# Optimization experiments

Hardware: AMD Instinct MI355X
Metric: run time of the kernel (lower is better)

## Reference

```python
import jax, jax.numpy as jnp
import numpy as np

D_MODEL = 1024
D_K = 1024
B, T = 4, 2048


def setup_inputs() -> dict:
    key = jax.random.key(0)
    kx, kq, kk, kv = jax.random.split(key, 4)
    s = 1.0 / np.sqrt(D_MODEL)
    return {
        "x": jax.random.normal(kx, (B, T, D_MODEL), dtype=jnp.float32),
        "W_q": jax.random.normal(kq, (D_MODEL, D_K), dtype=jnp.float32) * s,
        "W_k": jax.random.normal(kk, (D_MODEL, D_K), dtype=jnp.float32) * s,
        "W_v": jax.random.normal(kv, (D_MODEL, D_K), dtype=jnp.float32) * s,
    }


def reference(x, W_q, W_k, W_v):
    # x: (B, T, C); W_*: (C, d_k). Linear(no bias) == x @ W
    q = jnp.einsum('btc,ck->btk', x, W_q)
    k = jnp.einsum('btc,ck->btk', x, W_k)
    v = jnp.einsum('btc,ck->btk', x, W_v)
    d_k = W_q.shape[1]
    scores = jnp.einsum('bqk,bsk->bqs', q, k) / jnp.sqrt(jnp.asarray(d_k, x.dtype))
    T_ = x.shape[1]
    causal = jnp.tril(jnp.ones((T_, T_), dtype=bool))
    scores = jnp.where(causal, scores, jnp.asarray(-jnp.inf, scores.dtype))
    weights = jax.nn.softmax(scores, axis=-1)
    return jnp.einsum('bqs,bsk->bqk', weights, v)
```

## Files before the change

kernel.cpp:

```cpp
#include <hip/hip_runtime.h>
#include <hip/hip_bf16.h>
#include <stdint.h>
#include <math.h>

typedef __bf16 bf16x8 __attribute__((ext_vector_type(8)));
typedef float  f32x4  __attribute__((ext_vector_type(4)));
typedef unsigned int u32x4 __attribute__((ext_vector_type(4)));

__device__ __forceinline__ unsigned short f2bf(float x) {
    union { float f; unsigned u; } v; v.f = x;
    unsigned r = v.u + 0x7fffu + ((v.u >> 16) & 1u);
    return (unsigned short)(r >> 16);
}

__device__ __forceinline__ float bf2f(unsigned short b) {
    union { unsigned u; float f; } v; v.u = ((unsigned)b) << 16; return v.f;
}

__device__ __forceinline__ void async16(const void* g, void* l) {
    __builtin_amdgcn_global_load_lds(
        (const __attribute__((address_space(1))) void*)g,
        (__attribute__((address_space(3))) void*)l,
        16, 0, 0);
}

template <typename OutT, bool KLIMIT, bool VFOLD, int ZMODE, int TN>
__global__ __launch_bounds__(256, (TN == 128) ? 3 : 2) void gemm_bt(
    const unsigned short* __restrict__ A,
    const unsigned short* __restrict__ Bt,
    OutT* __restrict__ C,
    unsigned short* __restrict__ VtOut,
    int M, int N, int K, int lda, int ldb, int ldc,
    int ldvt, int nsplit,
    long long sA, long long sB, long long sC, long long sVt, float scale)
{
    constexpr int NJ   = TN / 32;
    constexpr int BUFE = (TN == 128) ? 8192 : 12288;

    int bn, bm, bz;
    if constexpr (ZMODE == 1) {
        const int o = blockIdx.x, x = o & 7, q = o >> 3;
        bz = x >> 1;
        const int tile = (x & 1) * 96 + q * 4 + blockIdx.z;
        bn = tile / 16; bm = tile % 16;
    } else if constexpr (ZMODE == 2) {
        const int o = blockIdx.x, x = o & 7, q = o >> 3;
        bz = x >> 1;
        const int t = (x & 1) * 68 + q * 4 + blockIdx.z;
        int r = (int)((sqrtf(8.f * (float)t + 1.f) - 1.f) * 0.5f);
        while ((r + 1) * (r + 2) / 2 <= t) r++;
        while (r * (r + 1) / 2 > t) r--;
        bm = r; bn = t - r * (r + 1) / 2;
    } else if constexpr (ZMODE == 3) {
        const int o = blockIdx.x, x = o & 7, q = o >> 3;
        bz = x >> 1;
        const int tile = (x & 1) * 64 + q * 4 + blockIdx.z;
        bn = tile >> 4; bm = 15 - (tile & 15);
    } else {
        bn = blockIdx.x; bm = blockIdx.y; bz = blockIdx.z;
    }

    A  += (long long)bz * sA;
    Bt += (long long)bz * sB;
    C  += (long long)bz * sC;

    const int m0 = bm * 128, n0 = bn * TN;
    const int Keff = KLIMIT ? min(K, (bm + 1) * 128) : K;
    const int nsteps = Keff >> 5;

    __shared__ __align__(16) unsigned short LDS[3 * BUFE];

    const int tid  = threadIdx.x;
    const int w    = tid >> 6, l = tid & 63;
    const int wr   = w >> 1,  wc = w & 1;
    const int lrow = l & 15,  quad = l >> 4;

    f32x4 acc[4][NJ] = {};

    const int cOff = (((l & 3) ^ ((l >> 3) & 3))) * 8;
    const unsigned short* aG0 = A + (long long)(m0 + 32 * w + (l >> 2))      * lda + cOff;
    const unsigned short* aG1 = A + (long long)(m0 + 32 * w + (l >> 2) + 16) * lda + cOff;
    const unsigned short* bG0 = Bt + (long long)(n0 + (TN / 4) * w + (l >> 2))      * ldb + cOff;
    const unsigned short* bG1 = Bt + (long long)(n0 + (TN / 4) * w + (l >> 2) + 16) * ldb + cOff;
    const unsigned short* bG2 = Bt + (long long)(n0 + (TN / 4) * w + (l >> 2) + 32) * ldb + cOff;
    const unsigned short* bG3 = Bt + (long long)(n0 + (TN / 4) * w + (l >> 2) + 48) * ldb + cOff;
    unsigned short* aL = &LDS[w * 1024 + l * 8];
    unsigned short* bL = &LDS[4096 + w * (TN * 8) + l * 8];

    const int sl = (lrow >> 1) & 3;

    auto STG = [&](int s) {
        const int off = (s % 3) * BUFE;
        const int kk  = s * 32;
        async16(aG0 + kk, aL + off);
        async16(aG1 + kk, aL + off + 512);
        async16(bG0 + kk, bL + off);
        async16(bG1 + kk, bL + off + 512);
        if constexpr (TN == 256) {
            async16(bG2 + kk, bL + off + 1024);
            async16(bG3 + kk, bL + off + 1536);
        }
    };

    STG(0);
    if (nsteps > 1) STG(1);

    for (int t = 0; t < nsteps; ++t) {
        if (t + 1 < nsteps) {
            if constexpr (TN == 128) asm volatile("s_waitcnt vmcnt(4)" ::: "memory");
            else                     asm volatile("s_waitcnt vmcnt(6)" ::: "memory");
        } else {
            asm volatile("s_waitcnt vmcnt(0)" ::: "memory");
        }
        __builtin_amdgcn_s_barrier();
        asm volatile("" ::: "memory");

        if (t + 2 < nsteps) STG(t + 2);

        const unsigned short* As = &LDS[(t % 3) * BUFE];
        const unsigned short* Bs = As + 4096;
        bf16x8 af[4], bfr[NJ];
#pragma unroll
        for (int i = 0; i < 4; i++)
            af[i]  = *(const bf16x8*)&As[(wr * 64 + i * 16 + lrow) * 32 + (quad ^ sl) * 8];
#pragma unroll
        for (int j = 0; j < NJ; j++)
            bfr[j] = *(const bf16x8*)&Bs[(wc * (TN / 2) + j * 16 + lrow) * 32 + (quad ^ sl) * 8];
#pragma unroll
        for (int i = 0; i < 4; i++)
#pragma unroll
            for (int j = 0; j < NJ; j++)
                acc[i][j] = __builtin_amdgcn_mfma_f32_16x16x32_bf16(af[i], bfr[j], acc[i][j], 0, 0, 0);
    }

    if constexpr (VFOLD) {
        if (n0 >= nsplit) {
            unsigned short* Vp = VtOut + (long long)bz * sVt;
#pragma unroll
            for (int i = 0; i < 4; i++) {
                const int t = m0 + wr * 64 + i * 16 + quad * 4;
#pragma unroll
                for (int j = 0; j < NJ; j++) {
                    const int d = (n0 - nsplit) + wc * (TN / 2) + j * 16 + lrow;
                    union { unsigned short u[4]; uint2 p; } o;
#pragma unroll
                    for (int r = 0; r < 4; r++) o.u[r] = f2bf(acc[i][j][r] * scale);
                    *(uint2*)(Vp + (long long)d * ldvt + t) = o.p;
                }
            }
            return;
        }
    }

    __syncthreads();

    const int erow = l >> 2, ep = l & 3;

    if constexpr (sizeof(OutT) == 2 && TN == 128) {
        char* eb = (char*)LDS + w * 2288;
#pragma unroll
        for (int i = 0; i < 4; i++) {
#pragma unroll
            for (int j = 0; j < 4; j++)
#pragma unroll
                for (int r = 0; r < 4; r++)
                    *(unsigned short*)(eb + (quad * 4 + r) * 144 + (j * 16 + lrow) * 2) =
                        f2bf(acc[i][j][r] * scale);
            const long long gm = m0 + wr * 64 + i * 16 + erow;
#pragma unroll
            for (int c = 0; c < 2; c++) {
                u32x4 d = *(u32x4*)(eb + erow * 144 + ep * 32 + c * 16);
                *(u32x4*)((unsigned short*)C + gm * ldc + (n0 + wc * 64 + ep * 16 + c * 8)) = d;
            }
        }
    } else if constexpr (sizeof(OutT) == 2 && TN == 256) {
        char* eb = (char*)LDS + w * 4352;
#pragma unroll
        for (int i = 0; i < 4; i++) {
#pragma unroll
            for (int j = 0; j < 8; j++)
#pragma unroll
                for (int r = 0; r < 4; r++)
                    *(unsigned short*)(eb + (quad * 4 + r) * 272 + (j * 16 + lrow) * 2) =
                        f2bf(acc[i][j][r] * scale);
            const long long gm = m0 + wr * 64 + i * 16 + erow;
#pragma unroll
            for (int c = 0; c < 4; c++) {
                u32x4 d = *(u32x4*)(eb + erow * 272 + ep * 64 + c * 16);
                *(u32x4*)((unsigned short*)C + gm * ldc + (n0 + wc * 128 + ep * 32 + c * 8)) = d;
            }
        }
    } else {
        char* eb = (char*)LDS + w * 2304;
#pragma unroll
        for (int i = 0; i < 4; i++) {
            const long long gm = m0 + wr * 64 + i * 16 + erow;
#pragma unroll
            for (int jc = 0; jc < NJ / 2; jc++) {
#pragma unroll
                for (int jj = 0; jj < 2; jj++)
#pragma unroll
                    for (int r = 0; r < 4; r++)
                        *(float*)(eb + (quad * 4 + r) * 144 + (jj * 16 + lrow) * 4) =
                            acc[i][2 * jc + jj][r] * scale;
#pragma unroll
                for (int c = 0; c < 2; c++) {
                    f32x4 d = *(f32x4*)(eb + erow * 144 + ep * 32 + c * 16);
                    *(f32x4*)((float*)C + gm * ldc + (n0 + wc * (TN / 2) + jc * 32 + ep * 8 + c * 4)) = d;
                }
            }
        }
    }
}

__global__ __launch_bounds__(256) void prep_fused(
    const float4* __restrict__ xin, unsigned short* __restrict__ xout, int n4, int nCast,
    const float* __restrict__ W0, const float* __restrict__ W1,
    const float* __restrict__ W2, unsigned short* __restrict__ wout, int n)
{
    const int tid = threadIdx.x;
    if ((int)blockIdx.x < nCast) {
        int i = blockIdx.x * 256 + tid;
        if (i >= n4) return;
        float4 v = xin[i];
        union { unsigned short u[4]; uint2 p; } o;
        o.u[0] = f2bf(v.x); o.u[1] = f2bf(v.y); o.u[2] = f2bf(v.z); o.u[3] = f2bf(v.w);
        *(uint2*)(xout + (long long)i * 4) = o.p;
        return;
    }
    const int bx = blockIdx.x - nCast;
    const int wz = bx >> 10, rem = bx & 1023;
    const int wy = rem >> 5, wx = rem & 31;
    const float* in = (wz == 0) ? W0 : (wz == 1) ? W1 : W2;
    unsigned short* out = wout + (long long)wz * n * n;
    __shared__ float tile[32][33];
    const int tx = tid & 31, ty = tid >> 5;
    const int c0 = wx * 32, r0 = wy * 32;
#pragma unroll
    for (int i = 0; i < 4; i++)
        tile[ty + i * 8][tx] = in[(long long)(r0 + ty + i * 8) * n + c0 + tx];
    __syncthreads();
#pragma unroll
    for (int i = 0; i < 4; i++)
        out[(long long)(c0 + ty + i * 8) * n + r0 + tx] = f2bf(tile[tx][ty + i * 8]);
}

__global__ __launch_bounds__(256) void causal_softmax_bf16(
    const unsigned short* __restrict__ S, unsigned short* __restrict__ P, int T)
{
    const int row = blockIdx.x;
    const int t   = row & (T - 1);
    const int L   = t + 1;
    const unsigned short* s = S + (long long)row * T;
    unsigned short* p = P + (long long)row * T;
    const int tid  = threadIdx.x;
    const int base = tid * 8;

    uint4 raw = *(const uint4*)(s + base);
    unsigned rr[4] = {raw.x, raw.y, raw.z, raw.w};
    float v[8];
#pragma unroll
    for (int k = 0; k < 4; k++) {
        union { unsigned u; float f; } a, b;
        a.u = (rr[k] & 0xFFFFu) << 16;
        b.u = rr[k] & 0xFFFF0000u;
        v[2 * k] = a.f; v[2 * k + 1] = b.f;
    }
    float mx = -3.0e38f;
#pragma unroll
    for (int k = 0; k < 8; k++) {
        if (base + k >= L) v[k] = -3.0e38f;
        mx = fmaxf(mx, v[k]);
    }
#pragma unroll
    for (int off = 32; off; off >>= 1) mx = fmaxf(mx, __shfl_xor(mx, off));
    __shared__ float red[4], red2[4];
    const int wid = tid >> 6, lid = tid & 63;
    if (lid == 0) red[wid] = mx;
    __syncthreads();
    mx = fmaxf(fmaxf(red[0], red[1]), fmaxf(red[2], red[3]));

    float sum = 0.f;
#pragma unroll
    for (int k = 0; k < 8; k++) { v[k] = __expf(v[k] - mx); sum += v[k]; }
#pragma unroll
    for (int off = 32; off; off >>= 1) sum += __shfl_xor(sum, off);
    if (lid == 0) red2[wid] = sum;
    __syncthreads();
    sum = red2[0] + red2[1] + red2[2] + red2[3];
    const float inv = 1.0f / sum;

    union { unsigned short u[8]; uint4 q; } o;
#pragma unroll
    for (int k = 0; k < 8; k++) o.u[k] = f2bf(v[k] * inv);
    *(uint4*)(p + base) = o.q;
}

extern "C" void kernel_launch(void* const* d_in, const int* in_sizes, int n_in,
                              void* d_out, int out_size, void* d_ws, size_t ws_size,
                              hipStream_t stream)
{
    const int B = 4, T = 2048, C = 1024, D = 1024;
    const float* x  = (const float*)d_in[0];
    const float* Wq = (const float*)d_in[1];
    const float* Wk = (const float*)d_in[2];
    const float* Wv = (const float*)d_in[3];
    float* out = (float*)d_out;
    char* ws = (char*)d_ws;

    const size_t MB = 1ull << 20;
    unsigned short* Xbf   = (unsigned short*)(ws + 0);
    unsigned short* WqkvT = (unsigned short*)(ws + 16 * MB);
    unsigned short* QK    = (unsigned short*)(ws + 22 * MB);
    unsigned short* Vt    = (unsigned short*)(ws + 54 * MB);
    unsigned short* Sbf   = (unsigned short*)(ws + 70 * MB);
    unsigned short* P     = (unsigned short*)(ws + 0);

    const long long sX  = (long long)T * C;
    const long long sQK = (long long)T * 2 * D;
    const long long sVt = (long long)D * T;
    const long long sS  = (long long)T * T;
    const long long sO  = (long long)T * D;

    {
        int n4 = B * T * C / 4;
        int nCast = (n4 + 255) / 256;
        prep_fused<<<dim3(nCast + 3072), dim3(256), 0, stream>>>(
            (const float4*)x, Xbf, n4, nCast, Wq, Wk, Wv, WqkvT, 1024);
    }
    {
        dim3 g(192, 1, 4), b(256);
        gemm_bt<unsigned short, false, true, 1, 256><<<g, b, 0, stream>>>(
            Xbf, WqkvT, QK, Vt, 2048, 3072, 1024, 1024, 1024, 2048,
             T,  2048, sX, 0, sQK, sVt, 1.0f);
    }
    {
        dim3 g(136, 1, 4), b(256);
        gemm_bt<unsigned short, false, false, 2, 128><<<g, b, 0, stream>>>(
            QK, QK + D, Sbf, nullptr, 2048, 2048, 1024, 2 * D, 2 * D, 2048,
            0, 0, sQK, sQK, sS, 0, 0.03125f);
    }
    {
        causal_softmax_bf16<<<dim3(B * T), dim3(256), 0, stream>>>(Sbf, P, T);
    }
    {
        dim3 g(128, 1, 4), b(256);
        gemm_bt<float, true, false, 3, 128><<<g, b, 0, stream>>>(
            P, Vt, out, nullptr, 2048, 1024, 2048, 2048, 2048, 1024,
            0, 0, sS, sVt, sO, 0, 1.0f);
    }
    (void)in_sizes; (void)n_in; (void)out_size; (void)ws_size;
}
```

Before: 235.5 us.

## Fuse causal softmax into QK GEMM epilogue and defer normalization to PV GEMM

```diff
diff --git a/kernel.cpp b/kernel.cpp
--- a/kernel.cpp
+++ b/kernel.cpp
@@ -24,12 +24,13 @@
         16, 0, 0);
 }
 
-template <typename OutT, bool KLIMIT, bool VFOLD, int ZMODE, int TN>
+template <typename OutT, bool KLIMIT, bool VFOLD, int ZMODE, int TN, int EPI>
 __global__ __launch_bounds__(256, (TN == 128) ? 3 : 2) void gemm_bt(
     const unsigned short* __restrict__ A,
     const unsigned short* __restrict__ Bt,
     OutT* __restrict__ C,
     unsigned short* __restrict__ VtOut,
+    float* __restrict__ RS,
     int M, int N, int K, int lda, int ldb, int ldc,
     int ldvt, int nsplit,
     long long sA, long long sB, long long sC, long long sVt, float scale)
@@ -69,11 +70,21 @@
     const int nsteps = Keff >> 5;
 
     __shared__ __align__(16) unsigned short LDS[3 * BUFE];
+    __shared__ float LDSI[128];
 
     const int tid  = threadIdx.x;
     const int w    = tid >> 6, l = tid & 63;
     const int wr   = w >> 1,  wc = w & 1;
     const int lrow = l & 15,  quad = l >> 4;
+
+    if constexpr (EPI == 2) {
+        if (tid < 128) {
+            const float* rp = RS + (long long)bz * 65536 + (m0 + tid);
+            float rs = 0.f;
+            for (int b = 0; b < 2 * (bm + 1); ++b) rs += rp[b * 2048];
+            LDSI[tid] = 1.0f / rs;
+        }
+    }
 
     f32x4 acc[4][NJ] = {};
 
@@ -156,7 +167,40 @@
 
     const int erow = l >> 2, ep = l & 3;
 
-    if constexpr (sizeof(OutT) == 2 && TN == 128) {
+    if constexpr (EPI == 1) {
+        char* eb = (char*)LDS + w * 2288;
+        float* rsp = RS + (long long)bz * 65536 + (bn * 2 + wc) * 2048;
+#pragma unroll
+        for (int i = 0; i < 4; i++) {
+            float ev[4][4];
+#pragma unroll
+            for (int j = 0; j < 4; j++)
+#pragma unroll
+                for (int r = 0; r < 4; r++) {
+                    const int grow = m0 + wr * 64 + i * 16 + quad * 4 + r;
+                    const int gcol = n0 + wc * 64 + j * 16 + lrow;
+                    float e = __expf(acc[i][j][r] * scale);
+                    e = (gcol <= grow) ? e : 0.f;
+                    const unsigned short qb = f2bf(e);
+                    ev[j][r] = bf2f(qb);
+                    *(unsigned short*)(eb + (quad * 4 + r) * 144 + (j * 16 + lrow) * 2) = qb;
+                }
+#pragma unroll
+            for (int r = 0; r < 4; r++) {
+                float p = ev[0][r] + ev[1][r] + ev[2][r] + ev[3][r];
+                p += __shfl_xor(p, 1); p += __shfl_xor(p, 2);
+                p += __shfl_xor(p, 4); p += __shfl_xor(p, 8);
+                if (lrow == 0)
+                    rsp[m0 + wr * 64 + i * 16 + quad * 4 + r] = p;
+            }
+            const long long gm = m0 + wr * 64 + i * 16 + erow;
+#pragma unroll
+            for (int c = 0; c < 2; c++) {
+                u32x4 d = *(u32x4*)(eb + erow * 144 + ep * 32 + c * 16);
+                *(u32x4*)((unsigned short*)C + gm * ldc + (n0 + wc * 64 + ep * 16 + c * 8)) = d;
+            }
+        }
+    } else if constexpr (sizeof(OutT) == 2 && TN == 128) {
         char* eb = (char*)LDS + w * 2288;
 #pragma unroll
         for (int i = 0; i < 4; i++) {
@@ -195,6 +239,8 @@
 #pragma unroll
         for (int i = 0; i < 4; i++) {
             const long long gm = m0 + wr * 64 + i * 16 + erow;
+            float inv = 1.0f;
+            if constexpr (EPI == 2) inv = LDSI[wr * 64 + i * 16 + erow];
 #pragma unroll
             for (int jc = 0; jc < NJ / 2; jc++) {
 #pragma unroll
@@ -206,6 +252,7 @@
 #pragma unroll
                 for (int c = 0; c < 2; c++) {
                     f32x4 d = *(f32x4*)(eb + erow * 144 + ep * 32 + c * 16);
+                    if constexpr (EPI == 2) d *= inv;
                     *(f32x4*)((float*)C + gm * ldc + (n0 + wc * (TN / 2) + jc * 32 + ep * 8 + c * 4)) = d;
                 }
             }
@@ -245,57 +292,6 @@
         out[(long long)(c0 + ty + i * 8) * n + r0 + tx] = f2bf(tile[tx][ty + i * 8]);
 }
 
-__global__ __launch_bounds__(256) void causal_softmax_bf16(
-    const unsigned short* __restrict__ S, unsigned short* __restrict__ P, int T)
-{
-    const int row = blockIdx.x;
-    const int t   = row & (T - 1);
-    const int L   = t + 1;
-    const unsigned short* s = S + (long long)row * T;
-    unsigned short* p = P + (long long)row * T;
-    const int tid  = threadIdx.x;
-    const int base = tid * 8;
-
-    uint4 raw = *(const uint4*)(s + base);
-    unsigned rr[4] = {raw.x, raw.y, raw.z, raw.w};
-    float v[8];
-#pragma unroll
-    for (int k = 0; k < 4; k++) {
-        union { unsigned u; float f; } a, b;
-        a.u = (rr[k] & 0xFFFFu) << 16;
-        b.u = rr[k] & 0xFFFF0000u;
-        v[2 * k] = a.f; v[2 * k + 1] = b.f;
-    }
-    float mx = -3.0e38f;
-#pragma unroll
-    for (int k = 0; k < 8; k++) {
-        if (base + k >= L) v[k] = -3.0e38f;
-        mx = fmaxf(mx, v[k]);
-    }
-#pragma unroll
-    for (int off = 32; off; off >>= 1) mx = fmaxf(mx, __shfl_xor(mx, off));
-    __shared__ float red[4], red2[4];
-    const int wid = tid >> 6, lid = tid & 63;
-    if (lid == 0) red[wid] = mx;
-    __syncthreads();
-    mx = fmaxf(fmaxf(red[0], red[1]), fmaxf(red[2], red[3]));
-
-    float sum = 0.f;
-#pragma unroll
-    for (int k = 0; k < 8; k++) { v[k] = __expf(v[k] - mx); sum += v[k]; }
-#pragma unroll
-    for (int off = 32; off; off >>= 1) sum += __shfl_xor(sum, off);
-    if (lid == 0) red2[wid] = sum;
-    __syncthreads();
-    sum = red2[0] + red2[1] + red2[2] + red2[3];
-    const float inv = 1.0f / sum;
-
-    union { unsigned short u[8]; uint4 q; } o;
-#pragma unroll
-    for (int k = 0; k < 8; k++) o.u[k] = f2bf(v[k] * inv);
-    *(uint4*)(p + base) = o.q;
-}
-
 extern "C" void kernel_launch(void* const* d_in, const int* in_sizes, int n_in,
                               void* d_out, int out_size, void* d_ws, size_t ws_size,
                               hipStream_t stream)
@@ -310,11 +306,11 @@
 
     const size_t MB = 1ull << 20;
     unsigned short* Xbf   = (unsigned short*)(ws + 0);
+    float*          RSP   = (float*)(ws + 0);
     unsigned short* WqkvT = (unsigned short*)(ws + 16 * MB);
     unsigned short* QK    = (unsigned short*)(ws + 22 * MB);
     unsigned short* Vt    = (unsigned short*)(ws + 54 * MB);
     unsigned short* Sbf   = (unsigned short*)(ws + 70 * MB);
-    unsigned short* P     = (unsigned short*)(ws + 0);
 
     const long long sX  = (long long)T * C;
     const long long sQK = (long long)T * 2 * D;
@@ -330,23 +326,20 @@
     }
     {
         dim3 g(192, 1, 4), b(256);
-        gemm_bt<unsigned short, false, true, 1, 256><<<g, b, 0, stream>>>(
-            Xbf, WqkvT, QK, Vt, 2048, 3072, 1024, 1024, 1024, 2048,
+        gemm_bt<unsigned short, false, true, 1, 256, 0><<<g, b, 0, stream>>>(
+            Xbf, WqkvT, QK, Vt, nullptr, 2048, 3072, 1024, 1024, 1024, 2048,
              T,  2048, sX, 0, sQK, sVt, 1.0f);
     }
     {
         dim3 g(136, 1, 4), b(256);
-        gemm_bt<unsigned short, false, false, 2, 128><<<g, b, 0, stream>>>(
-            QK, QK + D, Sbf, nullptr, 2048, 2048, 1024, 2 * D, 2 * D, 2048,
+        gemm_bt<unsigned short, false, false, 2, 128, 1><<<g, b, 0, stream>>>(
+            QK, QK + D, Sbf, nullptr, RSP, 2048, 2048, 1024, 2 * D, 2 * D, 2048,
             0, 0, sQK, sQK, sS, 0, 0.03125f);
-    }
-    {
-        causal_softmax_bf16<<<dim3(B * T), dim3(256), 0, stream>>>(Sbf, P, T);
     }
     {
         dim3 g(128, 1, 4), b(256);
-        gemm_bt<float, true, false, 3, 128><<<g, b, 0, stream>>>(
-            P, Vt, out, nullptr, 2048, 1024, 2048, 2048, 2048, 1024,
+        gemm_bt<float, true, false, 3, 128, 2><<<g, b, 0, stream>>>(
+            Sbf, Vt, out, nullptr, RSP, 2048, 1024, 2048, 2048, 2048, 1024,
             0, 0, sS, sVt, sO, 0, 1.0f);
     }
     (void)in_sizes; (void)n_in; (void)out_size; (void)ws_size;
```

Measured after the change: 247.7 us. 5.2% more time.
